# Optimization experiments

Hardware: AMD Instinct MI355X
Metric: run time of the kernel (lower is better)

## Reference

```python
import jax, jax.numpy as jnp
import numpy as np

N_HEAD = 16

def setup_inputs() -> dict:
    key = jax.random.key(0)
    ks = jax.random.split(key, 9)
    B, T, C = 4, 2048, 1024
    s = 1.0 / np.sqrt(C)
    return {
        "x":  jax.random.normal(ks[0], (B, T, C), jnp.float32),
        "Wq": jax.random.normal(ks[1], (C, C), jnp.float32) * s,
        "bq": jax.random.normal(ks[2], (C,), jnp.float32) * 0.02,
        "Wk": jax.random.normal(ks[3], (C, C), jnp.float32) * s,
        "bk": jax.random.normal(ks[4], (C,), jnp.float32) * 0.02,
        "Wv": jax.random.normal(ks[5], (C, C), jnp.float32) * s,
        "bv": jax.random.normal(ks[6], (C,), jnp.float32) * 0.02,
        "Wp": jax.random.normal(ks[7], (C, C), jnp.float32) * s,
        "bp": jax.random.normal(ks[8], (C,), jnp.float32) * 0.02,
    }

def reference(x, Wq, bq, Wk, bk, Wv, bv, Wp, bp):
    B, T, C = x.shape
    H, D = N_HEAD, C // N_HEAD
    # torch nn.Linear: y = x @ W^T + b
    q = (x @ Wq.T + bq).reshape(B, T, H, D).transpose(0, 2, 1, 3)  # [B,H,T,D]
    k = (x @ Wk.T + bk).reshape(B, T, H, D).transpose(0, 2, 1, 3)
    v = (x @ Wv.T + bv).reshape(B, T, H, D).transpose(0, 2, 1, 3)
    # full TxT causal attention (non-flash path)
    att = jnp.einsum('bhtd,bhsd->bhts', q, k) * (1.0 / np.sqrt(D))  # [B,H,T,T]
    causal = jnp.tril(jnp.ones((T, T), dtype=bool))
    att = jnp.where(causal[None, None], att, -jnp.inf)
    att = jax.nn.softmax(att, axis=-1)
    y = jnp.einsum('bhts,bhsd->bhtd', att, v)  # [B,H,T,D]
    y = y.transpose(0, 2, 1, 3).reshape(B, T, C)
    return y @ Wp.T + bp
```

## Files before the change

### kernel.cpp

```cpp
#include <hip/hip_runtime.h>

typedef __bf16 bf16_t;
typedef __bf16 bf16x8 __attribute__((ext_vector_type(8)));
typedef __bf16 bf16x4 __attribute__((ext_vector_type(4)));
typedef float f32x4 __attribute__((ext_vector_type(4)));
typedef unsigned short ushort_t;

#define T_SEQ 2048
#define C_DIM 1024
#define NH    16
#define HD    64

__device__ __forceinline__ ushort_t f2bf(float f) {
    unsigned u = __builtin_bit_cast(unsigned, f);
    u += 0x7FFFu + ((u >> 16) & 1u);
    return (ushort_t)(u >> 16);
}

#define X4  2097152
#define W4  262144
__global__ __launch_bounds__(256)
void cvt_all_kernel(const float* __restrict__ x,  const float* __restrict__ Wq,
                    const float* __restrict__ Wk, const float* __restrict__ Wv,
                    ushort_t* __restrict__ xb,  ushort_t* __restrict__ Wqb,
                    ushort_t* __restrict__ Wkb, ushort_t* __restrict__ Wvb) {
    int i = blockIdx.x * 256 + threadIdx.x;
    const float* src; ushort_t* dst; int off;
    if (i < X4)                { src = x;  dst = xb;  off = i; }
    else if (i < X4 + W4)      { src = Wq; dst = Wqb; off = i - X4; }
    else if (i < X4 + 2 * W4)  { src = Wk; dst = Wkb; off = i - X4 - W4; }
    else                       { src = Wv; dst = Wvb; off = i - X4 - 2 * W4; }
    float4 f = ((const float4*)src)[off];
    ushort4 u;
    u.x = f2bf(f.x); u.y = f2bf(f.y); u.z = f2bf(f.z); u.w = f2bf(f.w);
    ((ushort4*)dst)[off] = u;
}

template<bool AF32, bool BF32>
__device__ __forceinline__ void gemm_core_128(const void* __restrict__ Araw,
                                              const void* __restrict__ Braw,
                                              f32x4 (&acc)[4][4]) {
    __shared__ alignas(16) ushort_t As[128 * 72];
    __shared__ alignas(16) ushort_t Ws[128 * 72];
    const int tid  = threadIdx.x;
    const int lane = tid & 63;
    const int wv   = tid >> 6;
    const int wm   = wv >> 1, wn = wv & 1;
    const int quad = lane >> 4, ln = lane & 15;
    const int m0 = blockIdx.x * 128, n0 = blockIdx.y * 128;

    f32x4 z4 = {0.f, 0.f, 0.f, 0.f};
#pragma unroll
    for (int i = 0; i < 4; i++)
#pragma unroll
        for (int j = 0; j < 4; j++) acc[i][j] = z4;

    for (int kt = 0; kt < 1024; kt += 64) {
        if (AF32) {
            const float* A = (const float*)Araw;
#pragma unroll
            for (int p = 0; p < 8; ++p) {
                int cid = p * 256 + tid;
                int row = cid >> 4, c4 = (cid & 15) * 4;
                float4 f = *(const float4*)(A + (size_t)(m0 + row) * 1024 + kt + c4);
                ushort4 u;
                u.x = f2bf(f.x); u.y = f2bf(f.y); u.z = f2bf(f.z); u.w = f2bf(f.w);
                *(ushort4*)&As[row * 72 + c4] = u;
            }
        } else {
            const bf16_t* A = (const bf16_t*)Araw;
#pragma unroll
            for (int p = 0; p < 4; ++p) {
                int cid = p * 256 + tid;
                int row = cid >> 3, c8 = (cid & 7) * 8;
                *(uint4*)&As[row * 72 + c8] =
                    *(const uint4*)(A + (size_t)(m0 + row) * 1024 + kt + c8);
            }
        }
        if (BF32) {
            const float* Bm = (const float*)Braw;
#pragma unroll
            for (int p = 0; p < 8; ++p) {
                int cid = p * 256 + tid;
                int row = cid >> 4, c4 = (cid & 15) * 4;
                float4 f = *(const float4*)(Bm + (size_t)(n0 + row) * 1024 + kt + c4);
                ushort4 u;
                u.x = f2bf(f.x); u.y = f2bf(f.y); u.z = f2bf(f.z); u.w = f2bf(f.w);
                *(ushort4*)&Ws[row * 72 + c4] = u;
            }
        } else {
            const bf16_t* Bm = (const bf16_t*)Braw;
#pragma unroll
            for (int p = 0; p < 4; ++p) {
                int cid = p * 256 + tid;
                int row = cid >> 3, c8 = (cid & 7) * 8;
                *(uint4*)&Ws[row * 72 + c8] =
                    *(const uint4*)(Bm + (size_t)(n0 + row) * 1024 + kt + c8);
            }
        }
        __syncthreads();
#pragma unroll
        for (int ks = 0; ks < 2; ++ks) {
            bf16x8 af[4], bfr[4];
#pragma unroll
            for (int i = 0; i < 4; i++)
                af[i] = *(const bf16x8*)&As[(wm * 64 + i * 16 + ln) * 72 + ks * 32 + quad * 8];
#pragma unroll
            for (int j = 0; j < 4; j++)
                bfr[j] = *(const bf16x8*)&Ws[(wn * 64 + j * 16 + ln) * 72 + ks * 32 + quad * 8];
#pragma unroll
            for (int i = 0; i < 4; i++)
#pragma unroll
                for (int j = 0; j < 4; j++)
                    acc[i][j] = __builtin_amdgcn_mfma_f32_16x16x32_bf16(af[i], bfr[j],
                                                                        acc[i][j], 0, 0, 0);
        }
        __syncthreads();
    }
}

__global__ __launch_bounds__(256, 2)
void qkv_gemm_kernel(const bf16_t* __restrict__ xb,
                     const bf16_t* __restrict__ Wqb, const float* __restrict__ bq,
                     const bf16_t* __restrict__ Wkb, const float* __restrict__ bk,
                     const bf16_t* __restrict__ Wvb, const float* __restrict__ bv,
                     ushort_t* __restrict__ Qo, ushort_t* __restrict__ Ko,
                     ushort_t* __restrict__ Vo) {
    const int z = blockIdx.z;
    const bf16_t* W   = (z == 0) ? Wqb : (z == 1) ? Wkb : Wvb;
    const float* bias = (z == 0) ? bq : (z == 1) ? bk : bv;
    ushort_t* outp    = (z == 0) ? Qo : (z == 1) ? Ko : Vo;
    const float fs    = (z == 0) ? 0.18033688011112042f : 1.0f;

    f32x4 acc[4][4];
    gemm_core_128<false, false>(xb, W, acc);

    const int tid  = threadIdx.x;
    const int lane = tid & 63;
    const int wv2  = tid >> 6;
    const int wm   = wv2 >> 1, wn = wv2 & 1;
    const int quad = lane >> 4, ln = lane & 15;
    const int mbase = blockIdx.x * 128 + wm * 64;
    const int nbase = blockIdx.y * 128 + wn * 64;

#pragma unroll
    for (int j = 0; j < 4; j++) {
        int n = nbase + j * 16 + ln;
        float bj = bias[n];
        int h = n >> 6, d = n & 63;
#pragma unroll
        for (int i = 0; i < 4; i++) {
            int mr = mbase + i * 16 + quad * 4;
            int b = mr >> 11;
            int t = mr & 2047;
            if (z < 2) {
                ushort_t* op = outp + ((size_t)(b * NH + h) * T_SEQ + t) * HD + d;
#pragma unroll
                for (int r = 0; r < 4; r++)
                    op[(size_t)r * HD] = f2bf((acc[i][j][r] + bj) * fs);
            } else {
                ushort4 us;
                us.x = f2bf(acc[i][j][0] + bj);
                us.y = f2bf(acc[i][j][1] + bj);
                us.z = f2bf(acc[i][j][2] + bj);
                us.w = f2bf(acc[i][j][3] + bj);
                *(ushort4*)(outp + ((size_t)(b * NH + h) * HD + d) * T_SEQ + t) = us;
            }
        }
    }
}

__device__ __forceinline__ void qk_softmax(const ushort_t* __restrict__ Ks,
                                           bf16_t* __restrict__ PsW,
                                           bf16x8 aq0, bf16x8 aq1,
                                           bool diag, int wv, int quad, int ln) {
#pragma unroll
    for (int n16 = 0; n16 < 4; n16++) {
        f32x4 zz = {0.f, 0.f, 0.f, 0.f};
        bf16x8 bk0 = *(const bf16x8*)&Ks[(n16 * 16 + ln) * 72 + quad * 8];
        zz = __builtin_amdgcn_mfma_f32_16x16x32_bf16(bk0, aq0, zz, 0, 0, 0);
        bf16x8 bk1 = *(const bf16x8*)&Ks[(n16 * 16 + ln) * 72 + 32 + quad * 8];
        zz = __builtin_amdgcn_mfma_f32_16x16x32_bf16(bk1, aq1, zz, 0, 0, 0);
        bf16x4 pb;
#pragma unroll
        for (int r = 0; r < 4; r++) {
            float v = zz[r];
            v = (diag && (n16 * 16 + quad * 4 + r > wv * 16 + ln)) ? -1e30f : v;
            pb[r] = (bf16_t)__builtin_amdgcn_exp2f(v);
        }
        *(bf16x4*)&PsW[ln * 72 + n16 * 16 + quad * 4] = pb;
    }
}

__global__ __launch_bounds__(256, 4)
void flash_kernel(const ushort_t* __restrict__ Qw, const ushort_t* __restrict__ Kw,
                  const ushort_t* __restrict__ Vt, ushort_t* __restrict__ Y) {
    __shared__ alignas(16) ushort_t Ks[64 * 72];
    __shared__ alignas(16) ushort_t Vts[64 * 72];
    __shared__ alignas(16) bf16_t PsA[4 * 16 * 72];
    __shared__ alignas(16) bf16_t PsB[4 * 16 * 72];

    const int tid  = threadIdx.x;
    const int lane = tid & 63;
    const int wv   = tid >> 6;
    const int quad = lane >> 4, ln = lane & 15;
    const int L  = blockIdx.y * 16 + blockIdx.x;
    const int m  = L >> 3;
    const int bh = ((m >> 4) << 3) | (L & 7);
    const int p  = m & 15;
    const int qa = p, qb = 31 - p;
    const int b = bh >> 4, h = bh & 15;
    bf16_t* PsWA = &PsA[wv * 1152];
    bf16_t* PsWB = &PsB[wv * 1152];

    bf16x8 ones;
#pragma unroll
    for (int i = 0; i < 8; i++) ones[i] = (bf16_t)1.0f;

    const ushort_t* qpa = Qw + ((size_t)bh * T_SEQ + qa * 64 + wv * 16 + ln) * HD;
    const ushort_t* qpb = Qw + ((size_t)bh * T_SEQ + qb * 64 + wv * 16 + ln) * HD;
    bf16x8 aqA0 = *(const bf16x8*)(qpa + quad * 8);
    bf16x8 aqA1 = *(const bf16x8*)(qpa + 32 + quad * 8);
    bf16x8 aqB0 = *(const bf16x8*)(qpb + quad * 8);
    bf16x8 aqB1 = *(const bf16x8*)(qpb + 32 + quad * 8);

    f32x4 oA[4], oB[4];
    f32x4 z4 = {0.f, 0.f, 0.f, 0.f};
#pragma unroll
    for (int i = 0; i < 4; i++) { oA[i] = z4; oB[i] = z4; }
    f32x4 lA4 = z4, lB4 = z4;

    const int row0 = tid >> 3, c80 = (tid & 7) * 8;
    const int row1 = (256 + tid) >> 3, c81 = c80;

    uint4 pk0, pk1, pv0, pv1;
    pk0 = *(const uint4*)(Kw + ((size_t)bh * T_SEQ + row0) * HD + c80);
    pv0 = *(const uint4*)(Vt + ((size_t)bh * HD + row0) * T_SEQ + c80);
    pk1 = *(const uint4*)(Kw + ((size_t)bh * T_SEQ + row1) * HD + c81);
    pv1 = *(const uint4*)(Vt + ((size_t)bh * HD + row1) * T_SEQ + c81);

    for (int st = 0; st <= qb; ++st) {
        __syncthreads();
        *(uint4*)&Ks[row0 * 72 + c80]  = pk0;
        *(uint4*)&Vts[row0 * 72 + c80] = pv0;
        *(uint4*)&Ks[row1 * 72 + c81]  = pk1;
        *(uint4*)&Vts[row1 * 72 + c81] = pv1;
        if (st < qb) {
            int s1 = (st + 1) * 64;
            pk0 = *(const uint4*)(Kw + ((size_t)bh * T_SEQ + s1 + row0) * HD + c80);
            pv0 = *(const uint4*)(Vt + ((size_t)bh * HD + row0) * T_SEQ + s1 + c80);
            pk1 = *(const uint4*)(Kw + ((size_t)bh * T_SEQ + s1 + row1) * HD + c81);
            pv1 = *(const uint4*)(Vt + ((size_t)bh * HD + row1) * T_SEQ + s1 + c81);
        }
        __syncthreads();

        const bool doA = (st <= qa);
        if (doA)
            qk_softmax(Ks, PsWA, aqA0, aqA1, st == qa, wv, quad, ln);
        qk_softmax(Ks, PsWB, aqB0, aqB1, st == qb, wv, quad, ln);

#pragma unroll
        for (int ks = 0; ks < 2; ks++) {
            bf16x8 apA, apB;
            if (doA) {
                apA = *(const bf16x8*)&PsWA[ln * 72 + ks * 32 + quad * 8];
                lA4 = __builtin_amdgcn_mfma_f32_16x16x32_bf16(apA, ones, lA4, 0, 0, 0);
            }
            apB = *(const bf16x8*)&PsWB[ln * 72 + ks * 32 + quad * 8];
            lB4 = __builtin_amdgcn_mfma_f32_16x16x32_bf16(apB, ones, lB4, 0, 0, 0);
#pragma unroll
            for (int d16 = 0; d16 < 4; d16++) {
                bf16x8 bv = *(const bf16x8*)&Vts[(d16 * 16 + ln) * 72 + ks * 32 + quad * 8];
                if (doA)
                    oA[d16] = __builtin_amdgcn_mfma_f32_16x16x32_bf16(apA, bv, oA[d16], 0, 0, 0);
                oB[d16] = __builtin_amdgcn_mfma_f32_16x16x32_bf16(apB, bv, oB[d16], 0, 0, 0);
            }
        }
    }

#pragma unroll
    for (int ph = 0; ph < 2; ph++) {
        f32x4* o = ph ? oB : oA;
        f32x4 l4 = ph ? lB4 : lA4;
        int qt = ph ? qb : qa;
        f32x4 inv = {1.f / l4[0], 1.f / l4[1], 1.f / l4[2], 1.f / l4[3]};
        const int tg = qt * 64 + wv * 16 + quad * 4;
#pragma unroll
        for (int d16 = 0; d16 < 4; d16++) {
#pragma unroll
            for (int r = 0; r < 4; r++) {
                float v = o[d16][r] * inv[r];
                Y[((size_t)b * T_SEQ + tg + r) * C_DIM + h * HD + d16 * 16 + ln] = f2bf(v);
            }
        }
    }
}

__global__ __launch_bounds__(256, 2)
void proj_gemm_kernel(const bf16_t* __restrict__ Yw, const float* __restrict__ Wp,
                      const float* __restrict__ bp, float* __restrict__ out) {
    f32x4 acc[4][4];
    gemm_core_128<false, true>(Yw, Wp, acc);

    const int tid  = threadIdx.x;
    const int lane = tid & 63;
    const int wv2  = tid >> 6;
    const int wm   = wv2 >> 1, wn = wv2 & 1;
    const int quad = lane >> 4, ln = lane & 15;
    const int mbase = blockIdx.x * 128 + wm * 64;
    const int nbase = blockIdx.y * 128 + wn * 64;

#pragma unroll
    for (int j = 0; j < 4; j++) {
        int n = nbase + j * 16 + ln;
        float bj = bp[n];
#pragma unroll
        for (int i = 0; i < 4; i++) {
            int mr = mbase + i * 16 + quad * 4;
#pragma unroll
            for (int r = 0; r < 4; r++)
                out[(size_t)(mr + r) * C_DIM + n] = acc[i][j][r] + bj;
        }
    }
}

extern "C" void kernel_launch(void* const* d_in, const int* in_sizes, int n_in,
                              void* d_out, int out_size, void* d_ws, size_t ws_size,
                              hipStream_t stream) {
    const float* x  = (const float*)d_in[0];
    const float* Wq = (const float*)d_in[1];
    const float* bq = (const float*)d_in[2];
    const float* Wk = (const float*)d_in[3];
    const float* bk = (const float*)d_in[4];
    const float* Wv = (const float*)d_in[5];
    const float* bv = (const float*)d_in[6];
    const float* Wp = (const float*)d_in[7];
    const float* bp = (const float*)d_in[8];
    float* out = (float*)d_out;

    char* ws = (char*)d_ws;
    const size_t MB = (size_t)1 << 20;
    ushort_t* Qw = (ushort_t*)(ws);
    ushort_t* Kw = (ushort_t*)(ws + 16 * MB);
    ushort_t* Vt = (ushort_t*)(ws + 32 * MB);
    ushort_t* Yw = (ushort_t*)(ws + 48 * MB);

    ushort_t* xb  = (ushort_t*)out;
    ushort_t* Wqb = (ushort_t*)((char*)out + 16 * MB);
    ushort_t* Wkb = (ushort_t*)((char*)out + 18 * MB);
    ushort_t* Wvb = (ushort_t*)((char*)out + 20 * MB);

    cvt_all_kernel<<<11264, 256, 0, stream>>>(x, Wq, Wk, Wv, xb, Wqb, Wkb, Wvb);

    dim3 g1(64, 8, 3);
    qkv_gemm_kernel<<<g1, 256, 0, stream>>>((const bf16_t*)xb,
                                            (const bf16_t*)Wqb, bq,
                                            (const bf16_t*)Wkb, bk,
                                            (const bf16_t*)Wvb, bv,
                                            Qw, Kw, Vt);

    dim3 g2(16, 64);
    flash_kernel<<<g2, 256, 0, stream>>>(Qw, Kw, Vt, Yw);

    dim3 g3(64, 8, 1);
    proj_gemm_kernel<<<g3, 256, 0, stream>>>((const bf16_t*)Yw, Wp, bp, out);
}
```

Baseline: 265.3 us.

## Use async global-to-LDS loads with XOR swizzle in GEMMs; fuse dual QK softmax

The shared GEMM core now stages A and B tiles with global_load_lds async 16-byte copies into unpadded, XOR-swizzled LDS, which removes register round-trips and bank conflicts. Wp is converted to bf16 by a separate kernel after attention so the projection GEMM uses the same bf16 path. Both GEMMs raise the occupancy hint to 3 blocks per CU. The attention kernel merges the two per-tile QK+softmax calls into one function that shares the K fragment loads. The loop still has no double buffering, so load latency is exposed unless occupancy hides it.

```diff
diff --git a/kernel.cpp b/kernel.cpp
--- a/kernel.cpp
+++ b/kernel.cpp
@@ -15,6 +15,12 @@
     unsigned u = __builtin_bit_cast(unsigned, f);
     u += 0x7FFFu + ((u >> 16) & 1u);
     return (ushort_t)(u >> 16);
+}
+
+__device__ __forceinline__ void async_cp16(const void* g, void* l) {
+    __builtin_amdgcn_global_load_lds(
+        (const __attribute__((address_space(1))) void*)g,
+        (__attribute__((address_space(3))) void*)l, 16, 0, 0);
 }
 
 #define X4  2097152
@@ -36,12 +42,20 @@
     ((ushort4*)dst)[off] = u;
 }
 
-template<bool AF32, bool BF32>
-__device__ __forceinline__ void gemm_core_128(const void* __restrict__ Araw,
-                                              const void* __restrict__ Braw,
+__global__ __launch_bounds__(256)
+void cvt_wp_kernel(const float* __restrict__ Wp, ushort_t* __restrict__ Wpb) {
+    int i = blockIdx.x * 256 + threadIdx.x;
+    float4 f = ((const float4*)Wp)[i];
+    ushort4 u;
+    u.x = f2bf(f.x); u.y = f2bf(f.y); u.z = f2bf(f.z); u.w = f2bf(f.w);
+    ((ushort4*)Wpb)[i] = u;
+}
+
+__device__ __forceinline__ void gemm_core_128(const bf16_t* __restrict__ A,
+                                              const bf16_t* __restrict__ B,
                                               f32x4 (&acc)[4][4]) {
-    __shared__ alignas(16) ushort_t As[128 * 72];
-    __shared__ alignas(16) ushort_t Ws[128 * 72];
+    __shared__ alignas(16) ushort_t As[128 * 64];
+    __shared__ alignas(16) ushort_t Ws[128 * 64];
     const int tid  = threadIdx.x;
     const int lane = tid & 63;
     const int wv   = tid >> 6;
@@ -55,48 +69,16 @@
 #pragma unroll
         for (int j = 0; j < 4; j++) acc[i][j] = z4;
 
+    const int lr = lane >> 3;
+    const int lc = (lane & 7) ^ lr;
+    const bf16_t* Ab = A + (size_t)(m0 + wv * 32 + lr) * 1024 + lc * 8;
+    const bf16_t* Bb = B + (size_t)(n0 + wv * 32 + lr) * 1024 + lc * 8;
+
     for (int kt = 0; kt < 1024; kt += 64) {
-        if (AF32) {
-            const float* A = (const float*)Araw;
-#pragma unroll
-            for (int p = 0; p < 8; ++p) {
-                int cid = p * 256 + tid;
-                int row = cid >> 4, c4 = (cid & 15) * 4;
-                float4 f = *(const float4*)(A + (size_t)(m0 + row) * 1024 + kt + c4);
-                ushort4 u;
-                u.x = f2bf(f.x); u.y = f2bf(f.y); u.z = f2bf(f.z); u.w = f2bf(f.w);
-                *(ushort4*)&As[row * 72 + c4] = u;
-            }
-        } else {
-            const bf16_t* A = (const bf16_t*)Araw;
-#pragma unroll
-            for (int p = 0; p < 4; ++p) {
-                int cid = p * 256 + tid;
-                int row = cid >> 3, c8 = (cid & 7) * 8;
-                *(uint4*)&As[row * 72 + c8] =
-                    *(const uint4*)(A + (size_t)(m0 + row) * 1024 + kt + c8);
-            }
-        }
-        if (BF32) {
-            const float* Bm = (const float*)Braw;
-#pragma unroll
-            for (int p = 0; p < 8; ++p) {
-                int cid = p * 256 + tid;
-                int row = cid >> 4, c4 = (cid & 15) * 4;
-                float4 f = *(const float4*)(Bm + (size_t)(n0 + row) * 1024 + kt + c4);
-                ushort4 u;
-                u.x = f2bf(f.x); u.y = f2bf(f.y); u.z = f2bf(f.z); u.w = f2bf(f.w);
-                *(ushort4*)&Ws[row * 72 + c4] = u;
-            }
-        } else {
-            const bf16_t* Bm = (const bf16_t*)Braw;
-#pragma unroll
-            for (int p = 0; p < 4; ++p) {
-                int cid = p * 256 + tid;
-                int row = cid >> 3, c8 = (cid & 7) * 8;
-                *(uint4*)&Ws[row * 72 + c8] =
-                    *(const uint4*)(Bm + (size_t)(n0 + row) * 1024 + kt + c8);
-            }
+#pragma unroll
+        for (int p = 0; p < 4; ++p) {
+            async_cp16(Ab + (size_t)p * 8192 + kt, &As[(wv * 4 + p) * 512]);
+            async_cp16(Bb + (size_t)p * 8192 + kt, &Ws[(wv * 4 + p) * 512]);
         }
         __syncthreads();
 #pragma unroll
@@ -104,10 +86,12 @@
             bf16x8 af[4], bfr[4];
 #pragma unroll
             for (int i = 0; i < 4; i++)
-                af[i] = *(const bf16x8*)&As[(wm * 64 + i * 16 + ln) * 72 + ks * 32 + quad * 8];
+                af[i] = *(const bf16x8*)&As[(wm * 64 + i * 16 + ln) * 64 +
+                                            (((ks * 4 + quad) ^ (ln & 7)) * 8)];
 #pragma unroll
             for (int j = 0; j < 4; j++)
-                bfr[j] = *(const bf16x8*)&Ws[(wn * 64 + j * 16 + ln) * 72 + ks * 32 + quad * 8];
+                bfr[j] = *(const bf16x8*)&Ws[(wn * 64 + j * 16 + ln) * 64 +
+                                             (((ks * 4 + quad) ^ (ln & 7)) * 8)];
 #pragma unroll
             for (int i = 0; i < 4; i++)
 #pragma unroll
@@ -119,7 +103,7 @@
     }
 }
 
-__global__ __launch_bounds__(256, 2)
+__global__ __launch_bounds__(256, 3)
 void qkv_gemm_kernel(const bf16_t* __restrict__ xb,
                      const bf16_t* __restrict__ Wqb, const float* __restrict__ bq,
                      const bf16_t* __restrict__ Wkb, const float* __restrict__ bk,
@@ -133,7 +117,7 @@
     const float fs    = (z == 0) ? 0.18033688011112042f : 1.0f;
 
     f32x4 acc[4][4];
-    gemm_core_128<false, false>(xb, W, acc);
+    gemm_core_128(xb, W, acc);
 
     const int tid  = threadIdx.x;
     const int lane = tid & 63;
@@ -170,25 +154,41 @@
     }
 }
 
-__device__ __forceinline__ void qk_softmax(const ushort_t* __restrict__ Ks,
-                                           bf16_t* __restrict__ PsW,
-                                           bf16x8 aq0, bf16x8 aq1,
-                                           bool diag, int wv, int quad, int ln) {
+__device__ __forceinline__ void qk2_softmax(const ushort_t* __restrict__ Ks,
+                                            bf16_t* __restrict__ PsWA,
+                                            bf16_t* __restrict__ PsWB,
+                                            bf16x8 aqA0, bf16x8 aqA1,
+                                            bf16x8 aqB0, bf16x8 aqB1,
+                                            bool doA, bool diagA, bool diagB,
+                                            int wv, int quad, int ln) {
 #pragma unroll
     for (int n16 = 0; n16 < 4; n16++) {
-        f32x4 zz = {0.f, 0.f, 0.f, 0.f};
         bf16x8 bk0 = *(const bf16x8*)&Ks[(n16 * 16 + ln) * 72 + quad * 8];
-        zz = __builtin_amdgcn_mfma_f32_16x16x32_bf16(bk0, aq0, zz, 0, 0, 0);
         bf16x8 bk1 = *(const bf16x8*)&Ks[(n16 * 16 + ln) * 72 + 32 + quad * 8];
-        zz = __builtin_amdgcn_mfma_f32_16x16x32_bf16(bk1, aq1, zz, 0, 0, 0);
+        f32x4 zB = {0.f, 0.f, 0.f, 0.f};
+        zB = __builtin_amdgcn_mfma_f32_16x16x32_bf16(bk0, aqB0, zB, 0, 0, 0);
+        zB = __builtin_amdgcn_mfma_f32_16x16x32_bf16(bk1, aqB1, zB, 0, 0, 0);
+        if (doA) {
+            f32x4 zA = {0.f, 0.f, 0.f, 0.f};
+            zA = __builtin_amdgcn_mfma_f32_16x16x32_bf16(bk0, aqA0, zA, 0, 0, 0);
+            zA = __builtin_amdgcn_mfma_f32_16x16x32_bf16(bk1, aqA1, zA, 0, 0, 0);
+            bf16x4 pa;
+#pragma unroll
+            for (int r = 0; r < 4; r++) {
+                float v = zA[r];
+                v = (diagA && (n16 * 16 + quad * 4 + r > wv * 16 + ln)) ? -1e30f : v;
+                pa[r] = (bf16_t)__builtin_amdgcn_exp2f(v);
+            }
+            *(bf16x4*)&PsWA[ln * 72 + n16 * 16 + quad * 4] = pa;
+        }
         bf16x4 pb;
 #pragma unroll
         for (int r = 0; r < 4; r++) {
-            float v = zz[r];
-            v = (diag && (n16 * 16 + quad * 4 + r > wv * 16 + ln)) ? -1e30f : v;
+            float v = zB[r];
+            v = (diagB && (n16 * 16 + quad * 4 + r > wv * 16 + ln)) ? -1e30f : v;
             pb[r] = (bf16_t)__builtin_amdgcn_exp2f(v);
         }
-        *(bf16x4*)&PsW[ln * 72 + n16 * 16 + quad * 4] = pb;
+        *(bf16x4*)&PsWB[ln * 72 + n16 * 16 + quad * 4] = pb;
     }
 }
 
@@ -255,9 +255,8 @@
         __syncthreads();
 
         const bool doA = (st <= qa);
-        if (doA)
-            qk_softmax(Ks, PsWA, aqA0, aqA1, st == qa, wv, quad, ln);
-        qk_softmax(Ks, PsWB, aqB0, aqB1, st == qb, wv, quad, ln);
+        qk2_softmax(Ks, PsWA, PsWB, aqA0, aqA1, aqB0, aqB1,
+                    doA, st == qa, st == qb, wv, quad, ln);
 
 #pragma unroll
         for (int ks = 0; ks < 2; ks++) {
@@ -296,11 +295,11 @@
     }
 }
 
-__global__ __launch_bounds__(256, 2)
-void proj_gemm_kernel(const bf16_t* __restrict__ Yw, const float* __restrict__ Wp,
+__global__ __launch_bounds__(256, 3)
+void proj_gemm_kernel(const bf16_t* __restrict__ Yw, const bf16_t* __restrict__ Wpb,
                       const float* __restrict__ bp, float* __restrict__ out) {
     f32x4 acc[4][4];
-    gemm_core_128<false, true>(Yw, Wp, acc);
+    gemm_core_128(Yw, Wpb, acc);
 
     const int tid  = threadIdx.x;
     const int lane = tid & 63;
@@ -344,6 +343,7 @@
     ushort_t* Kw = (ushort_t*)(ws + 16 * MB);
     ushort_t* Vt = (ushort_t*)(ws + 32 * MB);
     ushort_t* Yw = (ushort_t*)(ws + 48 * MB);
+    ushort_t* Wpb = (ushort_t*)(ws);
 
     ushort_t* xb  = (ushort_t*)out;
     ushort_t* Wqb = (ushort_t*)((char*)out + 16 * MB);
@@ -362,6 +362,8 @@
     dim3 g2(16, 64);
     flash_kernel<<<g2, 256, 0, stream>>>(Qw, Kw, Vt, Yw);
 
+    cvt_wp_kernel<<<1024, 256, 0, stream>>>(Wp, Wpb);
+
     dim3 g3(64, 8, 1);
-    proj_gemm_kernel<<<g3, 256, 0, stream>>>((const bf16_t*)Yw, Wp, bp, out);
-}
+    proj_gemm_kernel<<<g3, 256, 0, stream>>>((const bf16_t*)Yw, (const bf16_t*)Wpb, bp, out);
+}
```

Result: faster. 248.4 us (-6.4%).
